# Kernel optimization log

Hardware: AMD Instinct MI355X
Metric: run time of the kernel (lower is better)

## Reference

```python
import jax, jax.numpy as jnp
import numpy as np

N = 1147      # 240 lncRNA + 412 disease + 495 miRNA nodes (hard-coded in source)
HID = 512
NH = 8        # heads
P = 73408     # edges (avg degree ~64)
IN_CH = 512


def _ln(x, eps=1e-5):
    m = x.mean(-1, keepdims=True)
    v = ((x - m) ** 2).mean(-1, keepdims=True)
    return (x - m) * jax.lax.rsqrt(v + eps)


def _seg_softmax_agg(logits, v_src, dst, n):
    # logits: [P, NH], v_src: [P, NH, d]; softmax over incoming edges per dst node
    m = jax.ops.segment_max(logits, dst, num_segments=n)
    m = jnp.where(jnp.isfinite(m), m, 0.0)
    a = jnp.exp(logits - m[dst])
    den = jax.ops.segment_sum(a, dst, num_segments=n)
    w = a / (den[dst] + 1e-9)
    return jax.ops.segment_sum(w[..., None] * v_src, dst, num_segments=n)


def _lap_pe(src, dst, n, k):
    # symmetric normalized Laplacian eigenvector positional encoding
    A = jnp.zeros((n, n), jnp.float32).at[src, dst].set(1.0)
    A = jnp.maximum(A, A.T)
    dinv = jax.lax.rsqrt(jnp.maximum(A.sum(1), 1.0))
    L = jnp.eye(n, dtype=jnp.float32) - dinv[:, None] * A * dinv[None, :]
    _, vecs = jnp.linalg.eigh(L)
    return vecs[:, 1:k + 1]  # drop trivial eigenvector


def _edge_layer(h, e, src, dst, Wq, Wk, Wv, We, Wo, Woe, Wfa, Wfb, Wea, Web):
    n, D = h.shape
    d = D // NH
    scale = 1.0 / np.sqrt(d)
    q = (h @ Wq).reshape(n, NH, d)
    k = (h @ Wk).reshape(n, NH, d)
    v = (h @ Wv).reshape(n, NH, d)
    ep = (e @ We).reshape(-1, NH, d)
    score = k[src] * q[dst] * scale * ep           # [P, NH, d]
    e1 = _ln(e + score.reshape(-1, D) @ Woe)       # edge residual path
    e1 = _ln(e1 + jax.nn.relu(e1 @ Wea) @ Web)
    agg = _seg_softmax_agg(score.sum(-1), v[src], dst, n).reshape(n, D)
    h1 = _ln(h + agg @ Wo)
    h1 = _ln(h1 + jax.nn.relu(h1 @ Wfa) @ Wfb)
    return h1, e1


def _gt_layer(h, src, dst, Wq, Wk, Wv, Wo, Wfa, Wfb):
    n, D = h.shape
    d = D // NH
    scale = 1.0 / np.sqrt(d)
    q = (h @ Wq).reshape(n, NH, d)
    k = (h @ Wk).reshape(n, NH, d)
    v = (h @ Wv).reshape(n, NH, d)
    logits = (k[src] * q[dst]).sum(-1) * scale     # [P, NH]
    agg = _seg_softmax_agg(logits, v[src], dst, n).reshape(n, D)
    h1 = _ln(h + agg @ Wo)
    h1 = _ln(h1 + jax.nn.relu(h1 @ Wfa) @ Wfb)
    return h1


def setup_inputs() -> dict:
    key = jax.random.key(0)
    ks = jax.random.split(key, 32)
    s = 0.02
    w = lambda i, shp: jax.random.normal(ks[i], shp, jnp.float32) * s
    return {
        'H': jax.random.normal(ks[0], (N, 1147), jnp.float32),
        'edge_w': jax.random.uniform(ks[1], (P, 1), jnp.float32),
        'edge_src': jax.random.randint(ks[2], (P,), 0, N, jnp.int32),
        'edge_dst': jax.random.randint(ks[3], (P,), 0, N, jnp.int32),
        'W_lin': w(4, (1147, IN_CH)), 'b_lin': jnp.zeros((IN_CH,), jnp.float32),
        'W_e': w(5, (1, HID)), 'b_e': jnp.zeros((HID,), jnp.float32),
        'W_h': w(6, (IN_CH, HID)), 'b_h': jnp.zeros((HID,), jnp.float32),
        'W_lap': w(7, (HID, HID)), 'b_lap': jnp.zeros((HID,), jnp.float32),
        'Wq1': w(8, (HID, HID)), 'Wk1': w(9, (HID, HID)), 'Wv1': w(10, (HID, HID)),
        'We1': w(11, (HID, HID)), 'Wo1': w(12, (HID, HID)), 'Woe1': w(13, (HID, HID)),
        'Wf1a': w(14, (HID, 2 * HID)), 'Wf1b': w(15, (2 * HID, HID)),
        'We1a': w(16, (HID, 2 * HID)), 'We1b': w(17, (2 * HID, HID)),
        'Wq2': w(18, (HID, HID)), 'Wk2': w(19, (HID, HID)), 'Wv2': w(20, (HID, HID)),
        'Wo2': w(21, (HID, HID)),
        'Wf2a': w(22, (HID, 2 * HID)), 'Wf2b': w(23, (2 * HID, HID)),
    }


def reference(H, edge_w, W_lin, b_lin, W_e, b_e, W_h, b_h, W_lap, b_lap,
              Wq1, Wk1, Wv1, We1, Wo1, Woe1, Wf1a, Wf1b, We1a, We1b,
              Wq2, Wk2, Wv2, Wo2, Wf2a, Wf2b, edge_src, edge_dst):
    e = edge_w @ W_e + b_e                       # embedding_e on edge weights
    h = (H @ W_lin + b_lin) @ W_h + b_h          # linear(1147->in_ch) then embedding_h
    pe = _lap_pe(edge_src, edge_dst, N, HID)     # laplacian positional encoding
    h = h + pe @ W_lap + b_lap
    z, _ = _edge_layer(h, e, edge_src, edge_dst, Wq1, Wk1, Wv1, We1,
                       Wo1, Woe1, Wf1a, Wf1b, We1a, We1b)
    z = _gt_layer(z, edge_src, edge_dst, Wq2, Wk2, Wv2, Wo2, Wf2a, Wf2b)
    return z  # [N, HID], already flat per node
```

## Files before the change

### kernel.cpp

```cpp
#include <hip/hip_runtime.h>
#include <hip/hip_cooperative_groups.h>
#include <math.h>

#define NN 1147
#define HID 512
#define LDAe 1152
#define LDQ 1152
#define LDD 1147
#define EPS32 5.9604644775390625e-08f
#define SAFMIN32 1.17549435e-38f
#define I0E 1026
#define TGRID 64
#define TBLK 1024
#define GENSTRIDE 16

struct EDMeta { int K; int nrot; int early; float rho; };
struct ETree { int st[64]; int sz[64]; int cnt; };
struct MergeLvl { int cnt; int st[32]; int n1[32]; int n2[32]; };

__device__ __forceinline__ float lapy2f(float x, float y){
  float xa=fabsf(x), ya=fabsf(y), w=fmaxf(xa,ya), z2=fminf(xa,ya);
  if (z2==0.f) return w;
  float q=z2/w; return w*sqrtf(1.f+q*q);
}
__device__ __forceinline__ void slartg(float ff, float gg, float* c, float* s, float* r){
  if (gg==0.f){ *c=1.f; *s=0.f; *r=ff; }
  else if (ff==0.f){ *c=0.f; *s=copysignf(1.f,gg); *r=fabsf(gg); }
  else {
    float d=sqrtf(ff*ff+gg*gg);
    *c=fabsf(ff)/d;
    *r=copysignf(d,ff);
    *s=gg/(*r);
  }
}
__device__ void slaev2(float a, float b, float cc, float* rt1, float* rt2, float* cs1, float* sn1){
  float sm=a+cc, df=a-cc, adf=fabsf(df), tb=b+b, ab=fabsf(tb);
  float acmx, acmn;
  if (fabsf(a)>fabsf(cc)){ acmx=a; acmn=cc; } else { acmx=cc; acmn=a; }
  float rt;
  if (adf>ab) rt=adf*sqrtf(1.f+(ab/adf)*(ab/adf));
  else if (adf<ab) rt=ab*sqrtf(1.f+(adf/ab)*(adf/ab));
  else rt=ab*sqrtf(2.f);
  int sgn1;
  if (sm<0.f){ *rt1=0.5f*(sm-rt); sgn1=-1; *rt2=(acmx/(*rt1))*acmn-(b/(*rt1))*b; }
  else if (sm>0.f){ *rt1=0.5f*(sm+rt); sgn1=1; *rt2=(acmx/(*rt1))*acmn-(b/(*rt1))*b; }
  else { *rt1=0.5f*rt; *rt2=-0.5f*rt; sgn1=1; }
  int sgn2; float cs;
  if (df>=0.f){ cs=df+rt; sgn2=1; } else { cs=df-rt; sgn2=-1; }
  float acs=fabsf(cs);
  if (acs>ab){ float ct=-tb/cs; *sn1=1.f/sqrtf(1.f+ct*ct); *cs1=ct*(*sn1); }
  else {
    if (ab==0.f){ *cs1=1.f; *sn1=0.f; }
    else { float tn=-cs/tb; *cs1=1.f/sqrtf(1.f+tn*tn); *sn1=tn*(*cs1); }
  }
  if (sgn1==sgn2){ float tn=*cs1; *cs1=-(*sn1); *sn1=tn; }
}
__device__ void lamrg0(int n1,int n2,const float* a,int dtrd1,int dtrd2,int* idx){
  int n1sv=n1,n2sv=n2;
  int ind1=(dtrd1>0)?0:(n1-1);
  int ind2=(dtrd2>0)?n1:(n1+n2-1);
  int i=0;
  while(n1sv>0&&n2sv>0){
    if(a[ind1]<=a[ind2]){idx[i++]=ind1;ind1+=dtrd1;n1sv--;}
    else{idx[i++]=ind2;ind2+=dtrd2;n2sv--;}
  }
  while(n2sv>0){idx[i++]=ind2;ind2+=dtrd2;n2sv--;}
  while(n1sv>0){idx[i++]=ind1;ind1+=dtrd1;n1sv--;}
}

__device__ __forceinline__ float tree256(float* red, float* bc, int tid){
  __syncthreads();
  if (tid<64){
    float b=(red[tid]+red[tid+128])+(red[tid+64]+red[tid+192]);
    b+=__shfl_down(b,32,64);
    b+=__shfl_down(b,16,64);
    b+=__shfl_down(b,8,64);
    b+=__shfl_down(b,4,64);
    b+=__shfl_down(b,2,64);
    b+=__shfl_down(b,1,64);
    if (tid==0) *bc=b;
  }
  __syncthreads();
  return *bc;
}

__global__ __launch_bounds__(256) void k_zero_f(float* p, int n){
  int i = blockIdx.x*256+threadIdx.x; if (i<n) p[i]=0.f;
}
__global__ __launch_bounds__(256) void k_zero_i(int* p, int n){
  int i = blockIdx.x*256+threadIdx.x; if (i<n) p[i]=0;
}

__global__ __launch_bounds__(256) void k_adj(const int* __restrict__ src, const int* __restrict__ dst,
                                             float* __restrict__ A, int P){
  int p = blockIdx.x*256+threadIdx.x;
  if (p>=P) return;
  int s=src[p], d=dst[p];
  A[(size_t)s*LDAe+d]=1.f;
  A[(size_t)d*LDAe+s]=1.f;
}
__global__ __launch_bounds__(256) void k_deg(const float* __restrict__ A, float* __restrict__ dinv){
  int row=blockIdx.x; int tid=threadIdx.x;
  __shared__ float red[256];
  float s=0.f;
  for (int c=tid;c<NN;c+=256) s+=A[(size_t)row*LDAe+c];
  red[tid]=s; __syncthreads();
  for(int st=128;st;st>>=1){ if(tid<st) red[tid]+=red[tid+st]; __syncthreads(); }
  if(tid==0) dinv[row]=1.f/sqrtf(fmaxf(red[0],1.f));
}
__global__ __launch_bounds__(256) void k_lap(float* __restrict__ A, const float* __restrict__ dinv){
  int row=blockIdx.y; int col=blockIdx.x*256+threadIdx.x;
  if (col>=NN) return;
  size_t idx=(size_t)row*LDAe+col;
  float v=A[idx];
  float v1=(dinv[row]*v)*dinv[col];
  float v2=(dinv[col]*v)*dinv[row];
  A[idx] = ((row==col)?1.f:0.f) - 0.5f*(v1+v2);
}

__device__ __forceinline__ float dload(const float* p){
  return __hip_atomic_load(p, __ATOMIC_RELAXED, __HIP_MEMORY_SCOPE_AGENT);
}
__device__ __forceinline__ void dstore(float* p, float v){
  __hip_atomic_store(p, v, __ATOMIC_RELAXED, __HIP_MEMORY_SCOPE_AGENT);
}

__device__ __forceinline__ void gbar(unsigned* flags, unsigned* genrep, unsigned tgt){
  __syncthreads();
  if (threadIdx.x==0)
    __hip_atomic_store(&flags[blockIdx.x], tgt, __ATOMIC_RELAXED, __HIP_MEMORY_SCOPE_AGENT);
  if (blockIdx.x==0){
    if (threadIdx.x<TGRID){
      while (__hip_atomic_load(&flags[threadIdx.x], __ATOMIC_RELAXED, __HIP_MEMORY_SCOPE_AGENT) < tgt)
        __builtin_amdgcn_s_sleep(1);
    }
    __syncthreads();
    if (threadIdx.x<TGRID)
      __hip_atomic_store(&genrep[threadIdx.x*GENSTRIDE], tgt, __ATOMIC_RELAXED, __HIP_MEMORY_SCOPE_AGENT);
  } else {
    if (threadIdx.x==0){
      while (__hip_atomic_load(&genrep[blockIdx.x*GENSTRIDE], __ATOMIC_RELAXED, __HIP_MEMORY_SCOPE_AGENT) < tgt)
        __builtin_amdgcn_s_sleep(1);
    }
    __syncthreads();
  }
}

__global__ __launch_bounds__(1024) void k_trid(float* __restrict__ A, float* __restrict__ evec,
    float* __restrict__ tauv, float* __restrict__ scalv, float* __restrict__ pv2,
    float* __restrict__ pub4, unsigned* __restrict__ flags, unsigned* __restrict__ genrep){
  __shared__ float vbuf[2][1152];
  __shared__ float pcur[1152];
  __shared__ float pubc[1152];
  __shared__ float red[256];
  __shared__ float bcv;
  int tid=threadIdx.x, bid=blockIdx.x;
  int wv=tid>>6, lane=tid&63;
  unsigned tgt=0;
  float tau, scal;
  {
    const float* row0=A;
    int m0=NN-1;
    if (tid<256){
      float s=0.f;
      for(int t=tid;t<m0-1;t+=256){ float x=row0[2+t]; s+=x*x; }
      red[tid]=s;
    }
    float xn2=tree256(red,&bcv,tid);
    float alpha=row0[1];
    float beta;
    if(xn2==0.f){ tau=0.f; beta=alpha; scal=0.f; }
    else { beta=-copysignf(sqrtf(alpha*alpha+xn2),alpha); tau=(beta-alpha)/beta; scal=1.f/(alpha-beta); }
    if(bid==0&&tid==0){ evec[0]=beta; tauv[0]=tau; scalv[0]=scal; }
    for(int t=tid;t<m0;t+=TBLK) vbuf[0][t]=row0[1+t];
    __syncthreads();
    for(int rr=0;rr<2;rr++){
      int r=16*bid+wv+rr*1024;
      if(r<1||r>=NN) continue;
      const float* arow=A+(size_t)r*LDAe+1;
      float acc=0.f;
      for(int c=lane;c<m0;c+=64){
        float v=(c==0)?1.f:vbuf[0][c]*scal;
        acc+=arow[c]*v;
      }
      for(int o=32;o;o>>=1) acc+=__shfl_down(acc,o,64);
      if(lane==0) dstore(&pv2[r],acc);
    }
    if(bid==0&&wv==1){
      const float* r1=A+(size_t)LDAe;
      for(int c=2+lane;c<NN;c+=64) dstore(&pub4[1280+c],r1[c]);
    }
  }
  gbar(flags,genrep,++tgt);
  int cur=0;
  for(int i=0;i<I0E;i++){
    if (bid>=8 && i>=16*bid+15){
      if (tid==0)
        __hip_atomic_store(&flags[bid], 0x7FFFFFFFu, __ATOMIC_RELAXED, __HIP_MEMORY_SCOPE_AGENT);
      return;
    }
    int m=NN-1-i, mp=m-1;
    float* vcur=vbuf[cur]; float* nxt=vbuf[cur^1];
    const float* pvs=pv2+(size_t)(i&1)*1280;
    const float* pbs=pub4+(size_t)((i+1)&3)*1280;
    if (tid<256){
      float s=0.f;
      for(int t=tid;t<m;t+=256){
        float pv=dload(&pvs[(i+1)+t]);
        pcur[t]=pv;
        float v=(t==0)?1.f:vcur[t]*scal;
        s+=pv*v;
      }
      red[tid]=s;
    } else {
      for(int t=tid-256;t<mp;t+=768) pubc[t]=dload(&pbs[(i+2)+t]);
    }
    float sv=tree256(red,&bcv,tid);
    float c2=tau*tau*sv*0.5f;
    const float vz=1.f;
    float wR0=tau*pcur[0]-c2*vz;
    if (tid<256){
      float s2=0.f;
      if (tid==0){
        float vC=vcur[1]*scal;
        float wC=tau*pcur[1]-c2*vC;
        nxt[0]=pubc[0]-(vz*wC+wR0*vC);
      }
      for(int u=tid+1;u<mp;u+=256){
        float vC=vcur[1+u]*scal;
        float wC=tau*pcur[1+u]-c2*vC;
        float x=pubc[u]-(vz*wC+wR0*vC);
        nxt[u]=x;
        s2+=x*x;
      }
      red[tid]=s2;
    }
    float xn2=tree256(red,&bcv,tid);
    float alpha1=nxt[0];
    float beta1,tau1,scal1;
    if(xn2==0.f){ tau1=0.f; beta1=alpha1; scal1=0.f; }
    else { beta1=-copysignf(sqrtf(alpha1*alpha1+xn2),alpha1); tau1=(beta1-alpha1)/beta1; scal1=1.f/(alpha1-beta1); }
    if(bid==0&&tid==0){ evec[i+1]=beta1; tauv[i+1]=tau1; scalv[i+1]=scal1; }
    float* pvd=pv2+(size_t)((i+1)&1)*1280;
    float* pbd=pub4+(size_t)((i+2)&3)*1280;
    for(int rr=0;rr<2;rr++){
      int r=16*bid+wv+rr*1024;
      if(r<i+1||r>=NN) continue;
      int tr=r-(i+1);
      float vR=(tr==0)?1.f:vcur[tr]*scal;
      float wR=tau*pcur[tr]-c2*vR;
      float* arow=A+(size_t)r*LDAe;
      if(lane==0) arow[i+1]=arow[i+1]-(vR*wR0+wR*vz);
      if(tr==0){
        for(int c=lane;c<mp;c+=64) arow[i+2+c]=nxt[c];
      } else {
        float acc=0.f;
        int ispub=(tr==1);
        for(int c=lane;c<mp;c+=64){
          float vC=vcur[1+c]*scal;
          float wC=tau*pcur[1+c]-c2*vC;
          float val=arow[i+2+c]-(vR*wC+wR*vC);
          arow[i+2+c]=val;
          float v1=(c==0)?1.f:nxt[c]*scal1;
          acc+=val*v1;
          if(ispub) dstore(&pbd[(i+2)+c],val);
        }
        for(int o=32;o;o>>=1) acc+=__shfl_down(acc,o,64);
        if(lane==0) dstore(&pvd[r],acc);
      }
    }
    gbar(flags,genrep,++tgt);
    cur^=1; tau=tau1; scal=scal1;
  }
}
__global__ __launch_bounds__(256) void k_tend(float* __restrict__ A, float* __restrict__ evec,
    float* __restrict__ tauv, float* __restrict__ scalv){
  __shared__ float T[121][122];
  __shared__ float red[256];
  __shared__ float bct;
  __shared__ float pl[121];
  __shared__ float el[121], tl[121], sl[121];
  __shared__ float sh3[2];
  int tid=threadIdx.x;
  for(int e=tid;e<121*121;e+=256){ int r=e/121,c=e%121; T[r][c]=A[(size_t)(I0E+r)*LDAe + I0E+c]; }
  __syncthreads();
  for(int li=0; li<120; ++li){
    int m=120-li;
    float s=0.f;
    for(int t=tid;t<m-1;t+=256){ float x=T[li][li+2+t]; s+=x*x; }
    red[tid]=s;
    float xn2t=tree256(red,&bct,tid);
    if(tid==0){
      float alpha=T[li][li+1], xn2=xn2t;
      float beta,tau,scal;
      if(xn2==0.f){ tau=0.f; beta=alpha; scal=0.f; }
      else { beta=-copysignf(sqrtf(alpha*alpha+xn2),alpha); tau=(beta-alpha)/beta; scal=1.f/(alpha-beta); }
      el[li]=beta; tl[li]=tau; sl[li]=scal;
      sh3[0]=tau; sh3[1]=scal;
    }
    __syncthreads();
    float tau=sh3[0], scal=sh3[1];
    if(tid<m){
      float acc=0.f;
      for(int c=0;c<m;c++){
        float v=(c==0)?1.f:T[li][li+1+c]*scal;
        acc+=T[li+1+tid][li+1+c]*v;
      }
      pl[tid]=acc;
    }
    __syncthreads();
    s=0.f;
    for(int t=tid;t<m;t+=256){
      float v=(t==0)?1.f:T[li][li+1+t]*scal;
      s+=pl[t]*v;
    }
    red[tid]=s;
    float sv=tree256(red,&bct,tid);
    float c2=tau*tau*sv*0.5f;
    for(int e=tid;e<m*m;e+=256){
      int r=e/m, c=e%m;
      float vR=(r==0)?1.f:T[li][li+1+r]*scal;
      float vC=(c==0)?1.f:T[li][li+1+c]*scal;
      float wR=tau*pl[r]-c2*vR;
      float wC=tau*pl[c]-c2*vC;
      T[li+1+r][li+1+c]-=vR*wC+wR*vC;
    }
    __syncthreads();
  }
  for(int e=tid;e<121*121;e+=256){ int r=e/121,c=e%121; A[(size_t)(I0E+r)*LDAe + I0E+c]=T[r][c]; }
  for(int t=tid;t<120;t+=256){ evec[I0E+t]=el[t]; tauv[I0E+t]=tl[t]; scalv[I0E+t]=sl[t]; }
}
__global__ __launch_bounds__(256) void k_harvest(const float* __restrict__ A, float* __restrict__ dv){
  int t=blockIdx.x*256+threadIdx.x;
  if (t<NN) dv[t]=A[(size_t)t*LDAe+t];
}

__global__ __launch_bounds__(256) void k_ed_scale(float* __restrict__ D, float* __restrict__ E){
  __shared__ float red[256];
  int tid=threadIdx.x;
  float m=0.f;
  for(int i=tid;i<NN;i+=256) m=fmaxf(m,fabsf(D[i]));
  for(int i=tid;i<NN-1;i+=256) m=fmaxf(m,fabsf(E[i]));
  red[tid]=m; __syncthreads();
  for(int s=128;s;s>>=1){ if(tid<s) red[tid]=fmaxf(red[tid],red[tid+s]); __syncthreads(); }
  float mul=1.f/red[0];
  __syncthreads();
  for(int i=tid;i<NN;i+=256) D[i]*=mul;
  for(int i=tid;i<NN-1;i+=256) E[i]*=mul;
}
__global__ void k_ed_cuts(float* D, const float* E, ETree t){
  int b=threadIdx.x;
  if (b==0||b>=t.cnt) return;
  int cut=t.st[b];
  float ae=fabsf(E[cut-1]);
  D[cut-1]-=ae; D[cut]-=ae;
}

__device__ void steqr1w(int n, float* d, float* e, float* z, int ldz, int lane){
  if (n<=1) return;
  const float eps=EPS32, eps2=EPS32*EPS32, safmin=SAFMIN32;
  float workc[32], works[32];
  int nmaxit=n*30, jtot=0;
  int l1=0;
  for(;;){
    if (l1>n-1) break;
    if (l1>0) e[l1-1]=0.f;
    int m;
    for(m=l1;m<n-1;m++){
      float tst=fabsf(e[m]);
      if (tst==0.f) break;
      if (tst<=(sqrtf(fabsf(d[m]))*sqrtf(fabsf(d[m+1])))*eps){ e[m]=0.f; break; }
    }
    int l=l1, lend=m, lsv=l, lendsv=lend;
    l1=m+1;
    if (lend==l) continue;
    float anorm=0.f;
    for(int i=l;i<=lend;i++) anorm=fmaxf(anorm,fabsf(d[i]));
    for(int i=l;i<lend;i++) anorm=fmaxf(anorm,fabsf(e[i]));
    if (anorm==0.f) continue;
    if (fabsf(d[lend])<fabsf(d[l])){ lend=lsv; l=lendsv; }
    float c,s,g,r,p,f,b,rt1,rt2;
    if (lend>l){
      for(;;){
        int mm;
        for(mm=l;mm<lend;mm++){
          float tst=e[mm]*e[mm];
          if (tst<=(eps2*fabsf(d[mm]))*fabsf(d[mm+1])+safmin) break;
        }
        if (mm<lend) e[mm]=0.f;
        p=d[l];
        if (mm==l){ d[l]=p; l++; if (l<=lend) continue; else break; }
        if (mm==l+1){
          slaev2(d[l],e[l],d[l+1],&rt1,&rt2,&c,&s);
          for(int row=lane;row<n;row+=64){
            float t1=z[(size_t)(l+1)*ldz+row];
            z[(size_t)(l+1)*ldz+row]=c*t1 - s*z[(size_t)l*ldz+row];
            z[(size_t)l*ldz+row]=s*t1 + c*z[(size_t)l*ldz+row];
          }
          d[l]=rt1; d[l+1]=rt2; e[l]=0.f;
          l+=2;
          if (l<=lend) continue; else break;
        }
        if (jtot==nmaxit) break;
        jtot++;
        g=(d[l+1]-p)/(2.f*e[l]);
        r=lapy2f(g,1.f);
        g=d[mm]-p+(e[l]/(g+copysignf(r,g)));
        s=1.f; c=1.f; p=0.f;
        for(int i=mm-1;i>=l;i--){
          f=s*e[i]; b=c*e[i];
          slartg(g,f,&c,&s,&r);
          if (i!=mm-1) e[i+1]=r;
          g=d[i+1]-p;
          r=(d[i]-g)*s+2.f*c*b;
          p=s*r;
          d[i+1]=g+p;
          g=c*r-b;
          workc[i-l]=c; works[i-l]=-s;
        }
        for(int j2=mm-1;j2>=l;j2--){
          float cc=workc[j2-l], ss2=works[j2-l];
          if (cc!=1.f||ss2!=0.f)
            for(int row=lane;row<n;row+=64){
              float t1=z[(size_t)(j2+1)*ldz+row];
              z[(size_t)(j2+1)*ldz+row]=cc*t1 - ss2*z[(size_t)j2*ldz+row];
              z[(size_t)j2*ldz+row]=ss2*t1 + cc*z[(size_t)j2*ldz+row];
            }
        }
        d[l]=d[l]-p;
        e[l]=g;
      }
    } else {
      for(;;){
        int mm;
        for(mm=l;mm>lend;mm--){
          float tst=e[mm-1]*e[mm-1];
          if (tst<=(eps2*fabsf(d[mm]))*fabsf(d[mm-1])+safmin) break;
        }
        if (mm>lend) e[mm-1]=0.f;
        p=d[l];
        if (mm==l){ d[l]=p; l--; if (l>=lend) continue; else break; }
        if (mm==l-1){
          slaev2(d[l-1],e[l-1],d[l],&rt1,&rt2,&c,&s);
          for(int row=lane;row<n;row+=64){
            float t1=z[(size_t)l*ldz+row];
            z[(size_t)l*ldz+row]=c*t1 - s*z[(size_t)(l-1)*ldz+row];
            z[(size_t)(l-1)*ldz+row]=s*t1 + c*z[(size_t)(l-1)*ldz+row];
          }
          d[l-1]=rt1; d[l]=rt2; e[l-1]=0.f;
          l-=2;
          if (l>=lend) continue; else break;
        }
        if (jtot==nmaxit) break;
        jtot++;
        g=(d[l-1]-p)/(2.f*e[l-1]);
        r=lapy2f(g,1.f);
        g=d[mm]-p+(e[l-1]/(g+copysignf(r,g)));
        s=1.f; c=1.f; p=0.f;
        for(int i=mm;i<=l-1;i++){
          f=s*e[i]; b=c*e[i];
          slartg(g,f,&c,&s,&r);
          if (i!=mm) e[i-1]=r;
          g=d[i]-p;
          r=(d[i+1]-g)*s+2.f*c*b;
          p=s*r;
          d[i]=g+p;
          g=c*r-b;
          workc[i-mm]=c; works[i-mm]=s;
        }
        for(int j2=mm;j2<=l-1;j2++){
          float cc=workc[j2-mm], ss2=works[j2-mm];
          if (cc!=1.f||ss2!=0.f)
            for(int row=lane;row<n;row+=64){
              float t1=z[(size_t)(j2+1)*ldz+row];
              z[(size_t)(j2+1)*ldz+row]=cc*t1 - ss2*z[(size_t)j2*ldz+row];
              z[(size_t)j2*ldz+row]=ss2*t1 + cc*z[(size_t)j2*ldz+row];
            }
        }
        d[l]=d[l]-p;
        e[l-1]=g;
      }
    }
  }
  for(int ii=1;ii<n;ii++){
    int i=ii-1,k=i; float pp=d[i];
    for(int j2=ii;j2<n;j2++) if (d[j2]<pp){k=j2;pp=d[j2];}
    if (k!=i){
      d[k]=d[i]; d[i]=pp;
      for(int row=lane;row<n;row+=64){
        float t1=z[(size_t)i*ldz+row];
        z[(size_t)i*ldz+row]=z[(size_t)k*ldz+row];
        z[(size_t)k*ldz+row]=t1;
      }
    }
  }
}
__global__ __launch_bounds__(64) void k_ed_leaves(float* D, float* E, float* QM, int* indxq, ETree t){
  int lf=blockIdx.x;
  if (lf>=t.cnt) return;
  int lane=threadIdx.x;
  int st=t.st[lf], n=t.sz[lf];
  __shared__ float dl[32], el[32];
  __shared__ float zloc[32][33];
  for(int i=lane;i<n;i+=64) dl[i]=D[st+i];
  for(int i=lane;i<n-1;i+=64) el[i]=E[st+i];
  for(int e=lane;e<n*n;e+=64){ int c=e/n, r=e%n; zloc[c][r]=(c==r)?1.f:0.f; }
  __syncthreads();
  steqr1w(n, dl, el, &zloc[0][0], 33, lane);
  __syncthreads();
  for(int i=lane;i<n;i+=64){ D[st+i]=dl[i]; indxq[st+i]=i; }
  for(int i=lane;i<n-1;i+=64) E[st+i]=el[i];
  for(int e=lane;e<n*n;e+=64){ int c=e/n, r=e%n; QM[(size_t)(st+c)*LDQ + st+r]=zloc[c][r]; }
}

__global__ __launch_bounds__(256) void k_ed_deflate2(float* __restrict__ D, int* __restrict__ indxq,
    float* __restrict__ dlamda, float* __restrict__ w, float* __restrict__ dstage,
    int* __restrict__ colmap, int* __restrict__ cmtype, int* __restrict__ indxcg,
    int* __restrict__ rotp, int* __restrict__ rotn, float* __restrict__ rotc, float* __restrict__ rots,
    EDMeta* __restrict__ meta, const float* __restrict__ QM, const float* __restrict__ E, MergeLvl lv){
  int mid=blockIdx.x; if(mid>=lv.cnt) return;
  int st=lv.st[mid], n1=lv.n1[mid], n2=lv.n2[mid], n=n1+n2;
  int tid=threadIdx.x;
  __shared__ float zl[1152], dl_[1152], dlam[1152], wl[1152], ds2[1152];
  __shared__ int iq[1152], im[1152], ix[1152], ixp[1152], ict[1152], is2[1152];
  __shared__ float rv[256]; __shared__ int ri[256];
  __shared__ float srho; __shared__ int sK, snrot, searly, simax, sjmax;
  float rr=E[st+n1-1];
  if(tid==0) srho=fabsf(2.f*rr);
  for(int i=tid;i<n;i+=256){
    float v = (i<n1)? QM[(size_t)(st+i)*LDQ + st+n1-1] : QM[(size_t)(st+i)*LDQ + st+n1];
    if(rr<0.f && i>=n1) v=-v;
    zl[i]=v*0.70710678118654752440f;
    dl_[i]=D[st+i];
    int q=indxq[st+i]; if(i>=n1) q+=n1;
    iq[i]=q;
    ict[i]=(i<n1)?1:3;
  }
  __syncthreads();
  {
    float bv=-1.f; int bi=0;
    for(int i2=tid;i2<n;i2+=256){ float a=fabsf(zl[i2]); if(a>bv){bv=a;bi=i2;} }
    rv[tid]=bv; ri[tid]=bi; __syncthreads();
    for(int stp=128;stp;stp>>=1){
      if(tid<stp){ if(rv[tid+stp]>rv[tid]||(rv[tid+stp]==rv[tid]&&ri[tid+stp]<ri[tid])){rv[tid]=rv[tid+stp];ri[tid]=ri[tid+stp];} }
      __syncthreads();
    }
    if(tid==0) simax=ri[0];
    __syncthreads();
  }
  {
    float bv=-1.f; int bi=0;
    for(int i2=tid;i2<n;i2+=256){ float a=fabsf(dl_[i2]); if(a>bv){bv=a;bi=i2;} }
    rv[tid]=bv; ri[tid]=bi; __syncthreads();
    for(int stp=128;stp;stp>>=1){
      if(tid<stp){ if(rv[tid+stp]>rv[tid]||(rv[tid+stp]==rv[tid]&&ri[tid+stp]<ri[tid])){rv[tid]=rv[tid+stp];ri[tid]=ri[tid+stp];} }
      __syncthreads();
    }
    if(tid==0) sjmax=ri[0];
    __syncthreads();
  }
  if(tid==0){
    for(int i=0;i<n;i++) dlam[i]=dl_[iq[i]];
    lamrg0(n1,n2,dlam,1,1,im);
    for(int i=0;i<n;i++) ix[i]=iq[im[i]];
    float tol=8.f*EPS32*fmaxf(fabsf(dl_[sjmax]),fabsf(zl[simax]));
    float rho=srho;
    int K=0,nrot=0,early=0;
    if(rho*fabsf(zl[simax])<=tol){
      early=1;
      for(int i=0;i<n;i++){ int s2=ix[i]; im[i]=s2; iq[i]=2; ds2[i]=dl_[s2]; is2[i]=i; }
    } else {
      int K2=n; int pj=0; int j=0;
      for(;j<n;j++){ int nj=ix[j]; if(rho*fabsf(zl[nj])<=tol){K2--;ict[nj]=4;ixp[K2]=nj;} else {pj=nj;break;} }
      for(j=j+1;;j++){
        if(j>=n) break;
        int nj=ix[j];
        if(rho*fabsf(zl[nj])<=tol){K2--;ict[nj]=4;ixp[K2]=nj;}
        else {
          float s=zl[pj], c=zl[nj];
          float tau2=lapy2f(c,s);
          float t=dl_[nj]-dl_[pj];
          c=c/tau2; s=-s/tau2;
          if(fabsf(t*c*s)<=tol){
            zl[nj]=tau2; zl[pj]=0.f;
            if(ict[nj]!=ict[pj]) ict[nj]=2;
            ict[pj]=4;
            rotp[st+nrot]=pj; rotn[st+nrot]=nj; rotc[st+nrot]=c; rots[st+nrot]=s; nrot++;
            float t2=dl_[pj]*c*c + dl_[nj]*s*s;
            dl_[nj]=dl_[pj]*s*s + dl_[nj]*c*c;
            dl_[pj]=t2;
            K2--;
            int i2=1;
            for(;;){
              if(K2+i2<=n-1 && dl_[pj]<dl_[ixp[K2+i2]]){ ixp[K2+i2-1]=ixp[K2+i2]; ixp[K2+i2]=pj; i2++; }
              else { ixp[K2+i2-1]=pj; break; }
            }
            pj=nj;
          } else {
            dlam[K]=dl_[pj]; wl[K]=zl[pj]; ixp[K]=pj; K++;
            pj=nj;
          }
        }
      }
      dlam[K]=dl_[pj]; wl[K]=zl[pj]; ixp[K]=pj; K++;
      int ctot[5]={0,0,0,0,0};
      for(int i=0;i<n;i++) ctot[ict[i]]++;
      int psm[5]; psm[1]=0; psm[2]=ctot[1]; psm[3]=psm[2]+ctot[2]; psm[4]=psm[3]+ctot[3];
      for(int jj=0;jj<n;jj++){
        int js=ixp[jj]; int ct=ict[js];
        int slot=psm[ct]++;
        im[slot]=js; is2[slot]=jj; ds2[slot]=dl_[js]; iq[slot]=ct;
      }
    }
    sK=K; snrot=nrot; searly=early;
  }
  __syncthreads();
  int K=sK;
  for(int i=tid;i<n;i+=256){
    colmap[st+i]=im[i];
    cmtype[st+i]=iq[i];
    indxcg[st+i]=is2[i];
    dstage[st+i]=ds2[i];
    if(i<K){ dlamda[st+i]=dlam[i]; w[st+i]=wl[i]; }
  }
  if(tid==0){ meta[mid].K=K; meta[mid].nrot=snrot; meta[mid].early=searly; meta[mid].rho=srho; }
}

__global__ __launch_bounds__(256) void k_ed_rot2(float* __restrict__ QM, const int* __restrict__ rotp,
    const int* __restrict__ rotn, const float* __restrict__ rotc, const float* __restrict__ rots,
    const EDMeta* __restrict__ meta, MergeLvl lv){
  int mid=blockIdx.y; if(mid>=lv.cnt) return;
  int st=lv.st[mid], n=lv.n1[mid]+lv.n2[mid];
  int row=blockIdx.x*256+threadIdx.x;
  if(row>=n) return;
  int nr=meta[mid].nrot;
  for(int k=0;k<nr;k++){
    size_t ip=(size_t)(st+rotp[st+k])*LDQ+st+row;
    size_t iq2=(size_t)(st+rotn[st+k])*LDQ+st+row;
    float c=rotc[st+k], s=rots[st+k];
    float x=QM[ip], y=QM[iq2];
    QM[ip]=c*x+s*y;
    QM[iq2]=c*y-s*x;
  }
}
__global__ __launch_bounds__(256) void k_ed_permute(const float* __restrict__ QM, float* __restrict__ Q2,
    const int* __restrict__ colmap, const int* __restrict__ cmtype, MergeLvl lv){
  int mid=blockIdx.z; if(mid>=lv.cnt) return;
  int st=lv.st[mid], n1=lv.n1[mid], n=n1+lv.n2[mid];
  int row=blockIdx.x*256+threadIdx.x;
  int slot=blockIdx.y;
  if(row>=n||slot>=n) return;
  int src=colmap[st+slot], ct=cmtype[st+slot];
  float v=QM[(size_t)(st+src)*LDQ + st+row];
  if(ct==1&&row>=n1) v=0.f;
  else if(ct==3&&row<n1) v=0.f;
  Q2[(size_t)(st+slot)*LDQ + st+row]=v;
}

// ... 348 lines not shown
    float* __restrict__ C0, float* __restrict__ C1, float* __restrict__ C2,
    int M, int Nc, int K){
  __shared__ float As[16][65];
  __shared__ float Bs[3][16][65];
  int bm=blockIdx.y*64, bn=blockIdx.x*64;
  int tid=threadIdx.x;
  int tr=tid/16, tc=tid%16;
  float acc[3][4][4]={};
  const float* Bp0=B0; const float* Bp1=B1; const float* Bp2=B2;
  for(int k0=0;k0<K;k0+=16){
    for(int l=0;l<4;l++){
      int e2=tid+l*256;
      int m_=e2/16, kk=e2%16;
      float av=0.f;
      if (bm+m_<M && k0+kk<K) av=A[(size_t)(bm+m_)*K + k0+kk];
      As[kk][m_]=av;
      int k2=e2/64, n2=e2%64;
      bool ok=(k0+k2<K && bn+n2<Nc);
      size_t bidx=(size_t)(k0+k2)*Nc + bn+n2;
      Bs[0][k2][n2]= ok? Bp0[bidx]:0.f;
      Bs[1][k2][n2]= ok? Bp1[bidx]:0.f;
      Bs[2][k2][n2]= ok? Bp2[bidx]:0.f;
    }
    __syncthreads();
    for(int kk=0;kk<16;kk++){
      float ar[4];
      #pragma unroll
      for(int i=0;i<4;i++) ar[i]=As[kk][tr*4+i];
      #pragma unroll
      for(int q=0;q<3;q++){
        float br[4];
        #pragma unroll
        for(int j=0;j<4;j++) br[j]=Bs[q][kk][tc*4+j];
        #pragma unroll
        for(int i=0;i<4;i++)
          #pragma unroll
          for(int j=0;j<4;j++) acc[q][i][j]+=ar[i]*br[j];
      }
    }
    __syncthreads();
  }
  for(int i=0;i<4;i++){
    int r=bm+tr*4+i;
    if (r>=M) continue;
    for(int j=0;j<4;j++){
      int c=bn+tc*4+j;
      if (c>=Nc) continue;
      C0[(size_t)r*Nc+c]=acc[0][i][j];
      C1[(size_t)r*Nc+c]=acc[1][i][j];
      C2[(size_t)r*Nc+c]=acc[2][i][j];
    }
  }
}

__global__ __launch_bounds__(256) void k_lnadd(const float* __restrict__ x, const float* __restrict__ y,
                                               float* __restrict__ out){
  int row=blockIdx.x; int tid=threadIdx.x;
  __shared__ float red[256];
  size_t base=(size_t)row*HID;
  float v0=x[base+tid]+y[base+tid];
  float v1=x[base+256+tid]+y[base+256+tid];
  red[tid]=v0+v1; __syncthreads();
  for(int st=128;st;st>>=1){ if(tid<st) red[tid]+=red[tid+st]; __syncthreads(); }
  float mean=red[0]*(1.f/512.f);
  __syncthreads();
  float d0=v0-mean, d1=v1-mean;
  red[tid]=d0*d0+d1*d1; __syncthreads();
  for(int st=128;st;st>>=1){ if(tid<st) red[tid]+=red[tid+st]; __syncthreads(); }
  float r=rsqrtf(red[0]*(1.f/512.f)+1e-5f);
  out[base+tid]=d0*r;
  out[base+256+tid]=d1*r;
}

__global__ __launch_bounds__(256) void k_prep_uw(const float* __restrict__ We, const float* __restrict__ be,
    const float* __restrict__ We1, float* __restrict__ u, float* __restrict__ w1){
  int c=blockIdx.x*256+threadIdx.x;
  if (c>=HID) return;
  float a=0.f,b=0.f;
  for(int f=0;f<HID;f++){ float m=We1[(size_t)f*HID+c]; a+=We[f]*m; b+=be[f]*m; }
  u[c]=a; w1[c]=b;
}

__global__ __launch_bounds__(256) void k_elogits(const float* __restrict__ q, const float* __restrict__ kk,
    const int* __restrict__ src, const int* __restrict__ dst, const float* __restrict__ ew,
    const float* __restrict__ uu, const float* __restrict__ ww, float* __restrict__ logit, int P, int useep){
  int gw=(blockIdx.x*256+threadIdx.x)>>6;
  int lane=threadIdx.x&63;
  if (gw>=P) return;
  int s=src[gw], d=dst[gw];
  const float* kr=kk+(size_t)s*HID;
  const float* qr=q+(size_t)d*HID;
  float a1[8], a2[8];
  #pragma unroll
  for(int j=0;j<8;j++){
    int c=j*64+lane;
    float prod=kr[c]*qr[c];
    if (useep){ a1[j]=prod*uu[c]; a2[j]=prod*ww[c]; }
    else { a1[j]=prod; a2[j]=0.f; }
  }
  #pragma unroll
  for(int o=32;o;o>>=1){
    #pragma unroll
    for(int j=0;j<8;j++){ a1[j]+=__shfl_down(a1[j],o,64); a2[j]+=__shfl_down(a2[j],o,64); }
  }
  if (lane==0){
    float w0 = useep? ew[gw] : 0.f;
    #pragma unroll
    for(int j=0;j<8;j++){
      float lg = useep ? 0.125f*(w0*a1[j]+a2[j]) : 0.125f*a1[j];
      logit[(size_t)gw*8+j]=lg;
    }
  }
}

__global__ __launch_bounds__(256) void k_count(const int* __restrict__ dst, int* __restrict__ cnt, int P){
  int p=blockIdx.x*256+threadIdx.x;
  if (p<P) atomicAdd(&cnt[dst[p]],1);
}
__global__ __launch_bounds__(256) void k_scan(const int* __restrict__ cnt, int* __restrict__ iptr){
  __shared__ int c[NN+1];
  int tid=threadIdx.x;
  for(int i=tid;i<NN;i+=256) c[i]=cnt[i];
  __syncthreads();
  if (tid==0){
    int s=0;
    for(int n=0;n<NN;n++){ int t=c[n]; c[n]=s; s+=t; }
    c[NN]=s;
  }
  __syncthreads();
  for(int i=tid;i<=NN;i+=256) iptr[i]=c[i];
}
__global__ __launch_bounds__(256) void k_fill(const int* __restrict__ dst, const int* __restrict__ iptr,
                                              int* __restrict__ iidx, int P){
  int n=blockIdx.x; int tid=threadIdx.x;
  int lane=tid&63, wv=tid>>6;
  __shared__ int wb[4]; __shared__ int scnt;
  if (tid==0) scnt=iptr[n];
  __syncthreads();
  for(int base=0;base<P;base+=256){
    int p=base+tid;
    bool f=(p<P)&&(dst[p]==n);
    unsigned long long m=__ballot(f);
    if (lane==0) wb[wv]=__popcll(m);
    __syncthreads();
    int off=0;
    #pragma unroll
    for(int i=0;i<4;i++) if (i<wv) off+=wb[i];
    if (f){
      int pre=__popcll(m & ((1ull<<lane)-1ull));
      iidx[scnt+off+pre]=p;
    }
    int tot=wb[0]+wb[1]+wb[2]+wb[3];
    __syncthreads();
    if (tid==0) scnt+=tot;
    __syncthreads();
  }
}

__global__ __launch_bounds__(256) void k_softmax(const float* __restrict__ logit, const int* __restrict__ iptr,
    const int* __restrict__ iidx, float* __restrict__ wght){
  int n=blockIdx.x; int tid=threadIdx.x;
  int beg=iptr[n], end=iptr[n+1];
  if (beg==end) return;
  __shared__ float red[256];
  __shared__ float smax[8], sden[8];
  float mx[8];
  #pragma unroll
  for(int h=0;h<8;h++) mx[h]=-1e30f;
  for(int t=beg+tid;t<end;t+=256){
    int e=iidx[t];
    #pragma unroll
    for(int h=0;h<8;h++) mx[h]=fmaxf(mx[h],logit[(size_t)e*8+h]);
  }
  for(int h=0;h<8;h++){
    red[tid]=mx[h]; __syncthreads();
    for(int st=128;st;st>>=1){ if(tid<st) red[tid]=fmaxf(red[tid],red[tid+st]); __syncthreads(); }
    if (tid==0) smax[h]=red[0];
    __syncthreads();
  }
  float sm[8];
  #pragma unroll
  for(int h=0;h<8;h++) sm[h]=0.f;
  for(int t=beg+tid;t<end;t+=256){
    int e=iidx[t];
    #pragma unroll
    for(int h=0;h<8;h++) sm[h]+=expf(logit[(size_t)e*8+h]-smax[h]);
  }
  for(int h=0;h<8;h++){
    red[tid]=sm[h]; __syncthreads();
    for(int st=128;st;st>>=1){ if(tid<st) red[tid]+=red[tid+st]; __syncthreads(); }
    if (tid==0) sden[h]=red[0];
    __syncthreads();
  }
  for(int t=beg+tid;t<end;t+=256){
    int e=iidx[t];
    #pragma unroll
    for(int h=0;h<8;h++) wght[(size_t)e*8+h]=expf(logit[(size_t)e*8+h]-smax[h])/(sden[h]+1e-9f);
  }
}

__global__ __launch_bounds__(512) void k_agg(const float* __restrict__ wght, const float* __restrict__ vv,
    const int* __restrict__ src, const int* __restrict__ iptr, const int* __restrict__ iidx,
    float* __restrict__ agg){
  int n=blockIdx.x; int c=threadIdx.x; int h=c>>6;
  int beg=iptr[n], end=iptr[n+1];
  float acc=0.f;
  for(int t=beg;t<end;++t){
    int e=iidx[t];
    acc += wght[(size_t)e*8+h]*vv[(size_t)src[e]*HID+c];
  }
  agg[(size_t)n*HID+c]=acc;
}

extern "C" void kernel_launch(void* const* d_in, const int* in_sizes, int n_in,
                              void* d_out, int out_size, void* d_ws, size_t ws_size,
                              hipStream_t stream){
  const float* H      = (const float*)d_in[0];
  const float* edge_w = (const float*)d_in[1];
  const int*   esrc   = (const int*)d_in[2];
  const int*   edst   = (const int*)d_in[3];
  const float* W_lin  = (const float*)d_in[4];
  const float* b_lin  = (const float*)d_in[5];
  const float* W_e    = (const float*)d_in[6];
  const float* b_e    = (const float*)d_in[7];
  const float* W_h    = (const float*)d_in[8];
  const float* b_h    = (const float*)d_in[9];
  const float* W_lap  = (const float*)d_in[10];
  const float* b_lap  = (const float*)d_in[11];
  const float* Wq1    = (const float*)d_in[12];
  const float* Wk1    = (const float*)d_in[13];
  const float* Wv1    = (const float*)d_in[14];
  const float* We1    = (const float*)d_in[15];
  const float* Wo1    = (const float*)d_in[16];
  const float* Wf1a   = (const float*)d_in[18];
  const float* Wf1b   = (const float*)d_in[19];
  const float* Wq2    = (const float*)d_in[22];
  const float* Wk2    = (const float*)d_in[23];
  const float* Wv2    = (const float*)d_in[24];
  const float* Wo2    = (const float*)d_in[25];
  const float* Wf2a   = (const float*)d_in[26];
  const float* Wf2b   = (const float*)d_in[27];
  const int P = in_sizes[1];
  float* out = (float*)d_out;

  char* base=(char*)d_ws;
  size_t off=0;
  auto AF=[&](size_t n)->float*{ float* r=(float*)(base+off); off+=((n*4+255)/256)*256; return r; };
  auto AI=[&](size_t n)->int*{ int* r=(int*)(base+off); off+=((n*4+255)/256)*256; return r; };
  const size_t SLOT=(size_t)NN*HID;
  float* A   = AF((size_t)NN*LDAe);
  float* QM  = AF((size_t)LDQ*NN);
  float* Q2  = AF((size_t)LDQ*NN);
  float* DC  = AF((size_t)LDD*LDD);
  float* dvec  = AF(1280);
  float* evec  = AF(1280);
  float* tauv  = AF(1280);
  float* scalv = AF(1280);
  float* pvec  = AF(1280);
  float* eddl  = AF(1280);
  float* edw   = AF(1280);
  float* edds  = AF(1280);
  float* rotc  = AF(1280);
  float* rots  = AF(1280);
  float* ub    = AF(512);
  float* w1b   = AF(512);
  float* pv2   = AF(2*1280);
  float* pub4  = AF(4*1280);
  int* indxq=AI(1280); int* edcm=AI(1280); int* edcmt=AI(1280); int* edic=AI(1280);
  int* rotp=AI(1280); int* rotn=AI(1280);
  EDMeta* meta=(EDMeta*)AI(192);
  int* icnt=AI(NN); int* iptr=AI(NN+1); int* iidx=AI(P);
  int* barws=AI(2048);
  unsigned* flags=(unsigned*)barws;
  unsigned* genrep=(unsigned*)(barws+64);
  (void)ws_size; (void)n_in; (void)out_size;

  float* W0=A;        float* W1=A+SLOT;
  float* W2=QM;       float* W3=QM+SLOT;
  float* W4=Q2;       float* W5=Q2+SLOT;
  float* W6=DC;       float* W7=DC+SLOT;
  (void)W7;
  float* Vt=W6;
  float* pe=W2;

  auto GEMM=[&](const float*Am,const float*Bm,const float*bias,const float*add,float*C,int M,int Nc,int K,int relu){
    dim3 g((Nc+63)/64,(M+63)/64);
    k_gemm<<<g,256,0,stream>>>(Am,Bm,bias,add,C,M,Nc,K,relu);
  };

  {
    int ntot=NN*LDAe;
    k_zero_f<<<(ntot+255)/256,256,0,stream>>>(A,ntot);
    k_adj<<<(P+255)/256,256,0,stream>>>(esrc,edst,A,P);
    k_deg<<<NN,256,0,stream>>>(A,pvec);
    dim3 g((NN+255)/256,NN);
    k_lap<<<g,256,0,stream>>>(A,pvec);
  }
  k_zero_i<<<8,256,0,stream>>>(barws,2048);
  {
    void* kargs[] = { (void*)&A, (void*)&evec, (void*)&tauv, (void*)&scalv,
                      (void*)&pv2, (void*)&pub4, (void*)&flags, (void*)&genrep };
    hipLaunchCooperativeKernel((const void*)k_trid, dim3(TGRID), dim3(TBLK), kargs, 0, stream);
  }
  k_tend<<<1,256,0,stream>>>(A,evec,tauv,scalv);
  k_harvest<<<(NN+255)/256,256,0,stream>>>(A,dvec);

  ETree tr;
  {
    int tmp[64]; tmp[0]=NN; int cnt=1;
    while (tmp[cnt-1]>25){
      for(int j2=cnt-1;j2>=0;j2--){ int p=tmp[j2]; tmp[2*j2]=p/2; tmp[2*j2+1]=p-p/2; }
      cnt*=2;
    }
    tr.cnt=cnt;
    int acc=0;
    for(int j2=0;j2<cnt;j2++){ tr.st[j2]=acc; tr.sz[j2]=tmp[j2]; acc+=tmp[j2]; }
  }
  k_ed_scale<<<1,256,0,stream>>>(dvec,evec);
  k_zero_f<<<(LDQ*NN+255)/256,256,0,stream>>>(QM,LDQ*NN);
  k_ed_cuts<<<1,64,0,stream>>>(dvec,evec,tr);
  k_ed_leaves<<<tr.cnt,64,0,stream>>>(dvec,evec,QM,indxq,tr);

  {
    int csz[64], cst[64], cn=tr.cnt;
    for(int i=0;i<cn;i++){ csz[i]=tr.sz[i]; cst[i]=tr.st[i]; }
    while (cn>1){
      MergeLvl lv; lv.cnt=cn/2;
      int maxn=0;
      for(int i=0;i<cn/2;i++){
        lv.st[i]=cst[2*i]; lv.n1[i]=csz[2*i]; lv.n2[i]=csz[2*i+1];
        int n=lv.n1[i]+lv.n2[i]; if(n>maxn) maxn=n;
      }
      k_ed_deflate2<<<lv.cnt,256,0,stream>>>(dvec,indxq,eddl,edw,edds,edcm,edcmt,edic,
                                             rotp,rotn,rotc,rots,meta,QM,evec,lv);
      { dim3 gr((maxn+255)/256,lv.cnt);
        k_ed_rot2<<<gr,256,0,stream>>>(QM,rotp,rotn,rotc,rots,meta,lv); }
      { dim3 gp((maxn+255)/256,maxn,lv.cnt);
        k_ed_permute<<<gp,256,0,stream>>>(QM,Q2,edcm,edcmt,lv); }
      { dim3 gs((maxn+63)/64,lv.cnt);
        k_ed_secular<<<gs,64,0,stream>>>(eddl,edw,meta,dvec,DC,lv);
        k_ed_lowner<<<gs,64,0,stream>>>(eddl,edw,DC,meta,lv); }
      { dim3 gv(maxn,lv.cnt);
        k_ed_vecs<<<gv,256,0,stream>>>(edw,DC,edic,meta,lv); }
      { dim3 gg((maxn+63)/64,(maxn+63)/64,lv.cnt);
        k_gemm_cm2<<<gg,256,0,stream>>>(Q2,DC,QM,meta,lv); }
      k_ed_post<<<lv.cnt,256,0,stream>>>(dvec,edds,indxq,meta,lv);
      for(int i=0;i<cn/2;i++){ cst[i]=cst[2*i]; csz[i]=csz[2*i]+csz[2*i+1]; }
      cn>>=1;
    }
  }
  { dim3 gg((NN+255)/256,512); k_ed_gather<<<gg,256,0,stream>>>(QM,indxq,Vt); }
  k_backt<<<256,128,0,stream>>>(A,tauv,scalv,Vt);
  { dim3 g((NN+31)/32,(512+31)/32); k_transpose<<<g,256,0,stream>>>(Vt,pe); }

  float* hx=W0; float* h0=W1; float* hb=W4;
  GEMM(H,W_lin,b_lin,nullptr,hx,NN,HID,NN,0);
  GEMM(hx,W_h,b_h,nullptr,h0,NN,HID,HID,0);
  GEMM(pe,W_lap,b_lap,h0,hb,NN,HID,HID,0);
  k_prep_uw<<<2,256,0,stream>>>(W_e,b_e,We1,ub,w1b);
  k_zero_i<<<(NN+255)/256,256,0,stream>>>(icnt,NN);
  k_count<<<(P+255)/256,256,0,stream>>>(edst,icnt,P);
  k_scan<<<1,256,0,stream>>>(icnt,iptr);
  k_fill<<<NN,256,0,stream>>>(edst,iptr,iidx,P);
  float* qb=W0; float* kb=W1; float* vb=W3;
  { dim3 g((HID+63)/64,(NN+63)/64);
    k_gemm3<<<g,256,0,stream>>>(hb,Wq1,Wk1,Wv1,qb,kb,vb,NN,HID,HID); }
  float* logit=W2;
  k_elogits<<<(P+3)/4,256,0,stream>>>(qb,kb,esrc,edst,edge_w,ub,w1b,logit,P,1);
  float* wght=W5;
  k_softmax<<<NN,256,0,stream>>>(logit,iptr,iidx,wght);
  float* aggb=W6;
  k_agg<<<NN,512,0,stream>>>(wght,vb,esrc,iptr,iidx,aggb);
  float* ob=W0;
  GEMM(aggb,Wo1,nullptr,nullptr,ob,NN,HID,HID,0);
  float* h1a=W3;
  k_lnadd<<<NN,256,0,stream>>>(hb,ob,h1a);
  float* tb1=W0;
  GEMM(h1a,Wf1a,nullptr,nullptr,tb1,NN,1024,HID,1);
  float* fb=W2;
  GEMM(tb1,Wf1b,nullptr,nullptr,fb,NN,HID,1024,0);
  float* h1=W5;
  k_lnadd<<<NN,256,0,stream>>>(h1a,fb,h1);
  float* q2=W0; float* k2=W1; float* v2=W2;
  { dim3 g((HID+63)/64,(NN+63)/64);
    k_gemm3<<<g,256,0,stream>>>(h1,Wq2,Wk2,Wv2,q2,k2,v2,NN,HID,HID); }
  float* logit2=W3;
  k_elogits<<<(P+3)/4,256,0,stream>>>(q2,k2,esrc,edst,nullptr,nullptr,nullptr,logit2,P,0);
  float* wght2=W4;
  k_softmax<<<NN,256,0,stream>>>(logit2,iptr,iidx,wght2);
  float* agg2=W6;
  k_agg<<<NN,512,0,stream>>>(wght2,v2,esrc,iptr,iidx,agg2);
  float* o2=W0;
  GEMM(agg2,Wo2,nullptr,nullptr,o2,NN,HID,HID,0);
  float* h2a=W1;
  k_lnadd<<<NN,256,0,stream>>>(h1,o2,h2a);
  float* tb2=W2;
  GEMM(h2a,Wf2a,nullptr,nullptr,tb2,NN,1024,HID,1);
  float* f2=W0;
  GEMM(tb2,Wf2b,nullptr,nullptr,f2,NN,HID,1024,0);
  k_lnadd<<<NN,256,0,stream>>>(h2a,f2,out);
}
```

Before: 28.30 ms.

## Finish late tridiagonalization steps in a single workgroup, fuse eigen prep kernels

The cooperative multi-block Householder tridiagonalization now stops at step 762. A new single-workgroup kernel runs the remaining steps up to 1026, keeping the broadcast vectors in shared memory and using __syncthreads instead of grid-wide barriers. This targets the cost of global barriers once the trailing matrix is small. The diagonal harvest, scaling and cut-adjust kernels are also merged into one launch. The trade-off is that a single workgroup uses far less of the GPU for steps that still touch up to about 384 rows.

After: 32.90 ms. +16.3%, slower.

```diff
diff --git a/kernel.cpp b/kernel.cpp
--- a/kernel.cpp
+++ b/kernel.cpp
@@ -9,6 +9,7 @@
 #define LDD 1147
 #define EPS32 5.9604644775390625e-08f
 #define SAFMIN32 1.17549435e-38f
+#define IMID 762
 #define I0E 1026
 #define TGRID 64
 #define TBLK 1024
@@ -193,7 +194,7 @@
   }
   gbar(flags,genrep,++tgt);
   int cur=0;
-  for(int i=0;i<I0E;i++){
+  for(int i=0;i<IMID;i++){
     if (bid>=8 && i>=16*bid+15){
       if (tid==0)
         __hip_atomic_store(&flags[bid], 0x7FFFFFFFu, __ATOMIC_RELAXED, __HIP_MEMORY_SCOPE_AGENT);
@@ -273,6 +274,99 @@
     cur^=1; tau=tau1; scal=scal1;
   }
 }
+
+__global__ __launch_bounds__(1024) void k_tmid(float* __restrict__ A, float* __restrict__ evec,
+    float* __restrict__ tauv, float* __restrict__ scalv,
+    const float* __restrict__ pv2, const float* __restrict__ pub4){
+  __shared__ float vbuf[2][1152];
+  __shared__ float pvl[2][1152];
+  __shared__ float pbl[4][1152];
+  __shared__ float red[256];
+  __shared__ float bcv;
+  int tid=threadIdx.x;
+  int wv=tid>>6, lane=tid&63;
+  int cur=IMID&1;
+  float tau=tauv[IMID], scal=scalv[IMID];
+  {
+    int m0=NN-1-IMID;
+    const float* rowv=A+(size_t)IMID*LDAe+(IMID+1);
+    for(int t=tid;t<m0;t+=TBLK) vbuf[cur][t]=rowv[t];
+    const float* pvs=pv2+(size_t)(IMID&1)*1280;
+    for(int t=tid;t<m0;t+=TBLK) pvl[IMID&1][(IMID+1)+t]=pvs[(IMID+1)+t];
+    const float* pbs=pub4+(size_t)((IMID+1)&3)*1280;
+    for(int t=tid;t<m0-1;t+=TBLK) pbl[(IMID+1)&3][(IMID+2)+t]=pbs[(IMID+2)+t];
+  }
+  __syncthreads();
+  for(int i=IMID;i<I0E;i++){
+    int m=NN-1-i, mp=m-1;
+    float* vcur=vbuf[cur]; float* nxt=vbuf[cur^1];
+    float* pvs=pvl[i&1];
+    float* pbs=pbl[(i+1)&3];
+    if (tid<256){
+      float s=0.f;
+      for(int t=tid;t<m;t+=256){
+        float pv=pvs[(i+1)+t];
+        float v=(t==0)?1.f:vcur[t]*scal;
+        s+=pv*v;
+      }
+      red[tid]=s;
+    }
+    float sv=tree256(red,&bcv,tid);
+    float c2=tau*tau*sv*0.5f;
+    const float vz=1.f;
+    float wR0=tau*pvs[i+1]-c2*vz;
+    if (tid<256){
+      float s2=0.f;
+      if (tid==0){
+        float vC=vcur[1]*scal;
+        float wC=tau*pvs[(i+1)+1]-c2*vC;
+        nxt[0]=pbs[(i+2)]-(vz*wC+wR0*vC);
+      }
+      for(int u=tid+1;u<mp;u+=256){
+        float vC=vcur[1+u]*scal;
+        float wC=tau*pvs[(i+1)+1+u]-c2*vC;
+        float x=pbs[(i+2)+u]-(vz*wC+wR0*vC);
+        nxt[u]=x;
+        s2+=x*x;
+      }
+      red[tid]=s2;
+    }
+    float xn2=tree256(red,&bcv,tid);
+    float alpha1=nxt[0];
+    float beta1,tau1,scal1;
+    if(xn2==0.f){ tau1=0.f; beta1=alpha1; scal1=0.f; }
+    else { beta1=-copysignf(sqrtf(alpha1*alpha1+xn2),alpha1); tau1=(beta1-alpha1)/beta1; scal1=1.f/(alpha1-beta1); }
+    if(tid==0){ evec[i+1]=beta1; tauv[i+1]=tau1; scalv[i+1]=scal1; }
+    float* pvd=pvl[(i+1)&1];
+    float* pbd=pbl[(i+2)&3];
+    for(int r=i+1+wv; r<NN; r+=16){
+      int tr=r-(i+1);
+      float vR=(tr==0)?1.f:vcur[tr]*scal;
+      float wR=tau*pvs[(i+1)+tr]-c2*vR;
+      float* arow=A+(size_t)r*LDAe;
+      if(lane==0) arow[i+1]=arow[i+1]-(vR*wR0+wR*vz);
+      if(tr==0){
+        for(int c=lane;c<mp;c+=64) arow[i+2+c]=nxt[c];
+      } else {
+        float acc=0.f;
+        int ispub=(tr==1);
+        for(int c=lane;c<mp;c+=64){
+          float vC=vcur[1+c]*scal;
+          float wC=tau*pvs[(i+1)+1+c]-c2*vC;
+          float val=arow[i+2+c]-(vR*wC+wR*vC);
+          arow[i+2+c]=val;
+          float v1=(c==0)?1.f:nxt[c]*scal1;
+          acc+=val*v1;
+          if(ispub) pbd[(i+2)+c]=val;
+        }
+        for(int o=32;o;o>>=1) acc+=__shfl_down(acc,o,64);
+        if(lane==0) pvd[r]=acc;
+      }
+    }
+    __syncthreads();
+    cur^=1; tau=tau1; scal=scal1;
+  }
+}
 __global__ __launch_bounds__(256) void k_tend(float* __restrict__ A, float* __restrict__ evec,
     float* __restrict__ tauv, float* __restrict__ scalv){
   __shared__ float T[121][122];
@@ -330,14 +424,13 @@
   for(int e=tid;e<121*121;e+=256){ int r=e/121,c=e%121; A[(size_t)(I0E+r)*LDAe + I0E+c]=T[r][c]; }
   for(int t=tid;t<120;t+=256){ evec[I0E+t]=el[t]; tauv[I0E+t]=tl[t]; scalv[I0E+t]=sl[t]; }
 }
-__global__ __launch_bounds__(256) void k_harvest(const float* __restrict__ A, float* __restrict__ dv){
-  int t=blockIdx.x*256+threadIdx.x;
-  if (t<NN) dv[t]=A[(size_t)t*LDAe+t];
-}
-
-__global__ __launch_bounds__(256) void k_ed_scale(float* __restrict__ D, float* __restrict__ E){
+
+__global__ __launch_bounds__(256) void k_prep_ed(const float* __restrict__ A, float* __restrict__ D,
+                                                 float* __restrict__ E, ETree t){
   __shared__ float red[256];
   int tid=threadIdx.x;
+  for(int i=tid;i<NN;i+=256) D[i]=A[(size_t)i*LDAe+i];
+  __syncthreads();
   float m=0.f;
   for(int i=tid;i<NN;i+=256) m=fmaxf(m,fabsf(D[i]));
   for(int i=tid;i<NN-1;i+=256) m=fmaxf(m,fabsf(E[i]));
@@ -347,13 +440,12 @@
   __syncthreads();
   for(int i=tid;i<NN;i+=256) D[i]*=mul;
   for(int i=tid;i<NN-1;i+=256) E[i]*=mul;
-}
-__global__ void k_ed_cuts(float* D, const float* E, ETree t){
-  int b=threadIdx.x;
-  if (b==0||b>=t.cnt) return;
-  int cut=t.st[b];
-  float ae=fabsf(E[cut-1]);
-  D[cut-1]-=ae; D[cut]-=ae;
+  __syncthreads();
+  if (tid>0 && tid<t.cnt){
+    int cut=t.st[tid];
+    float ae=fabsf(E[cut-1]);
+    D[cut-1]-=ae; D[cut]-=ae;
+  }
 }
 
 __device__ void steqr1w(int n, float* d, float* e, float* z, int ldz, int lane){
@@ -1308,8 +1400,8 @@
                       (void*)&pv2, (void*)&pub4, (void*)&flags, (void*)&genrep };
     hipLaunchCooperativeKernel((const void*)k_trid, dim3(TGRID), dim3(TBLK), kargs, 0, stream);
   }
+  k_tmid<<<1,TBLK,0,stream>>>(A,evec,tauv,scalv,pv2,pub4);
   k_tend<<<1,256,0,stream>>>(A,evec,tauv,scalv);
-  k_harvest<<<(NN+255)/256,256,0,stream>>>(A,dvec);
 
   ETree tr;
   {
@@ -1322,9 +1414,8 @@
     int acc=0;
     for(int j2=0;j2<cnt;j2++){ tr.st[j2]=acc; tr.sz[j2]=tmp[j2]; acc+=tmp[j2]; }
   }
-  k_ed_scale<<<1,256,0,stream>>>(dvec,evec);
+  k_prep_ed<<<1,256,0,stream>>>(A,dvec,evec,tr);
   k_zero_f<<<(LDQ*NN+255)/256,256,0,stream>>>(QM,LDQ*NN);
-  k_ed_cuts<<<1,64,0,stream>>>(dvec,evec,tr);
   k_ed_leaves<<<tr.cnt,64,0,stream>>>(dvec,evec,QM,indxq,tr);
 
   {
```
